# Kernel tuning notes

Hardware: AMD Instinct MI355X
Metric: run time of the kernel (lower is better)

## Reference

```python
import jax, jax.numpy as jnp
import numpy as np

N_NODES = 50000
N_EDGES = 400000
N_GRAPHS = 512
F = 32        # num_features
NB = 32       # mp_num_basis_fn
ZMAX = 118
CUTOFF = 5.0
NSPH = 9      # (mp_max_degree+1)^2 with max_degree=2
DEG_IDX = jnp.array([0, 1, 1, 1, 2, 2, 2, 2, 2])  # degree of each spherical component


def _bernstein(u, n=NB):
    # reciprocal_bernstein radial basis: Bernstein polynomials of degree n-1 at u in [0,1)
    k = jnp.arange(n, dtype=jnp.float32)
    log_binom = (jax.scipy.special.gammaln(float(n)) - jax.scipy.special.gammaln(k + 1.0)
                 - jax.scipy.special.gammaln(float(n) - k))
    u = jnp.clip(u, 1e-7, 1.0 - 1e-7)[..., None]
    return jnp.exp(log_binom + k * jnp.log(u) + (float(n) - 1.0 - k) * jnp.log1p(-u))


def _smooth_cutoff(r, cutoff=CUTOFF):
    t = r / cutoff
    return jnp.where(t < 1.0, jnp.exp(1.0 - 1.0 / jnp.clip(1.0 - t * t, 1e-7, None)), 0.0)


def _sph(u):
    # real spherical harmonics (cartesian normalization) up to degree 2; u: (E,3) unit vectors
    x, y, z = u[:, 0], u[:, 1], u[:, 2]
    c = jnp.sqrt(jnp.float32(3.0))
    return jnp.stack([jnp.ones_like(x), y, z, x,
                      c * x * y, c * y * z, 0.5 * (3.0 * z * z - 1.0),
                      c * z * x, 0.5 * c * (x * x - y * y)], axis=-1)


def _dense(x, W, b):
    # equivariant Dense: shared kernel over spherical components, bias only on scalar (l=0)
    y = jnp.einsum('nmf,fg->nmg', x, W)
    return y.at[:, 0, :].add(b)


def _silu_gate(x):
    # equivariant silu: scalar channel gates all degrees (scalar part -> exact silu)
    return x * jax.nn.sigmoid(x[:, 0:1, :])


def setup_inputs() -> dict:
    key = jax.random.key(0)
    ks = jax.random.split(key, 24)
    s = 1.0 / np.sqrt(F)
    sb = 1.0 / np.sqrt(NB)
    inp = {
        'positions': 2.0 * jax.random.normal(ks[0], (N_NODES, 3), jnp.float32),
        'embed': jax.random.normal(ks[1], (ZMAX, F), jnp.float32),
        'Wy0': sb * jax.random.normal(ks[2], (3, NB, F), jnp.float32),
        'Wx0': sb * jax.random.normal(ks[3], (3, NB, F), jnp.float32),
        'W1_0': s * jax.random.normal(ks[4], (F, F), jnp.float32),
        'b1_0': jnp.zeros((F,), jnp.float32),
        'W2_0': s * jax.random.normal(ks[5], (F, F), jnp.float32),
        'b2_0': jnp.zeros((F,), jnp.float32),
        'c0': jnp.full((1,), 0.5, jnp.float32),
        'Wr_last': sb * jax.random.normal(ks[6], (NB, F), jnp.float32),
        'W1_1': s * jax.random.normal(ks[7], (F, F), jnp.float32),
        'b1_1': jnp.zeros((F,), jnp.float32),
        'W2_1': s * jax.random.normal(ks[8], (F, F), jnp.float32),
        'b2_1': jnp.zeros((F,), jnp.float32),
        'c1': jnp.full((1,), 0.5, jnp.float32),
        'Wro1': s * jax.random.normal(ks[9], (F, F), jnp.float32),
        'bro1': jnp.zeros((F,), jnp.float32),
        'Wro2': s * jax.random.normal(ks[10], (F, 1), jnp.float32),
        'bro2': jnp.zeros((1,), jnp.float32),
        'atomic_bias': jax.random.normal(ks[11], (ZMAX,), jnp.float32),
        'atomic_numbers': jax.random.randint(ks[12], (N_NODES,), 0, ZMAX, jnp.int32),
        'dst_idx': jax.random.randint(ks[13], (N_EDGES,), 0, N_NODES, jnp.int32),
        'src_idx': jax.random.randint(ks[14], (N_EDGES,), 0, N_NODES, jnp.int32),
        'batch_segments': jnp.sort(jax.random.randint(ks[15], (N_NODES,), 0, N_GRAPHS, jnp.int32)),
        'graph_mask': jnp.ones((N_GRAPHS,), jnp.bool_),
    }
    return inp


def reference(positions, embed, Wy0, Wx0, W1_0, b1_0, W2_0, b2_0, c0,
              Wr_last, W1_1, b1_1, W2_1, b2_1, c1,
              Wro1, bro1, Wro2, bro2, atomic_bias,
              atomic_numbers, dst_idx, src_idx, batch_segments, graph_mask):
    # --- edge geometry (gather_src/gather_dst) ---
    disp = positions[src_idx] - positions[dst_idx]                # (E,3)
    r = jnp.sqrt(jnp.sum(disp * disp, axis=-1) + 1e-12)           # (E,)
    u = disp / r[:, None]
    Y = _sph(u)                                                   # (E,9)
    rbf = _bernstein(r / (r + 1.0)) * _smooth_cutoff(r)[:, None]  # (E,NB)

    # --- atomic embedding, lifted to (N, 9, F) with zero higher degrees ---
    x0 = embed[atomic_numbers]                                    # (N,F)
    x = jnp.concatenate([x0[:, None, :], jnp.zeros((N_NODES, NSPH - 1, F), x0.dtype)], axis=1)

    # --- iteration 0: full-degree equivariant message pass ---
    wy = jnp.einsum('eb,lbf->elf', rbf, Wy0)[:, DEG_IDX, :]       # (E,9,F) radial weights, (0,l)->l path
    wx = jnp.einsum('eb,lbf->elf', rbf, Wx0)[:, DEG_IDX, :]       # (l,0)->l path
    xs = x[src_idx]                                               # (E,9,F)
    msg = wy * Y[:, :, None] * xs[:, 0:1, :] + wx * xs
    y = jax.ops.segment_sum(msg, dst_idx, num_segments=N_NODES)   # (N,9,F)
    y = x + y
    y = _silu_gate(_dense(y, W1_0, b1_0))
    y = _dense(y, W2_0, b2_0)
    x = x + jax.nn.silu(c0) * y                                   # y_nl == 0 (era disabled)

    # --- iteration 1 (last): max_degree=0 message pass, then reduce to scalars ---
    w0 = rbf @ Wr_last                                            # (E,F)
    msg0 = w0 * x[src_idx, 0, :]
    y0 = jax.ops.segment_sum(msg0, dst_idx, num_segments=N_NODES) # (N,F)
    xs0 = x[:, 0, :]                                              # change_max_degree -> scalars
    y0 = xs0 + y0
    y0 = jax.nn.silu(y0 @ W1_1 + b1_1)
    y0 = y0 @ W2_1 + b2_1
    xs0 = xs0 + jax.nn.silu(c1) * y0

    # --- atomic readout and per-graph sum ---
    h = jax.nn.silu(xs0 @ Wro1 + bro1)
    e_atom = (h @ Wro2)[:, 0] + bro2[0] + atomic_bias[atomic_numbers]
    e_graph = jax.ops.segment_sum(e_atom, batch_segments, num_segments=N_GRAPHS)
    return jnp.where(graph_mask, e_graph, 0.0)
```

## Files before the change

kernel.cpp:

```cpp
#include <hip/hip_runtime.h>
#include <math.h>

#define NNODES 50000
#define NEDGES 400000
#define NGRAPHS 512
#define FDIM 32
#define CAP 32

static constexpr float BINOM31[32] = {
    1.f, 31.f, 465.f, 4495.f, 31465.f, 169911.f, 736281.f, 2629575.f,
    7888725.f, 20160075.f, 44352165.f, 84672315.f, 141120525.f, 206253075.f,
    265182525.f, 300540195.f, 300540195.f, 265182525.f, 206253075.f,
    141120525.f, 84672315.f, 44352165.f, 20160075.f, 7888725.f, 2629575.f,
    736281.f, 169911.f, 31465.f, 4495.f, 465.f, 31.f, 1.f
};

__device__ __forceinline__ float fast_rcp(float x) {
    return __builtin_amdgcn_rcpf(x);
}
__device__ __forceinline__ float silu(float x) {
    return x * fast_rcp(1.0f + __expf(-x));
}

__global__ __launch_bounds__(256) void prep(
    const float* __restrict__ pos,
    const float* __restrict__ Wy0, const float* __restrict__ Wx0,
    const float* __restrict__ Wr_last,
    float4* __restrict__ pos4, int* __restrict__ deg,
    float* __restrict__ out,
    float* __restrict__ cwA, float* __restrict__ cwB)
{
    int i = blockIdx.x * 256 + threadIdx.x;
    if (i < NGRAPHS) out[i] = 0.0f;
    if (i < FDIM * FDIM) {
        float b = BINOM31[i >> 5];
        cwA[i] = b * (Wy0[i] + Wx0[i]);
        cwB[i] = b * Wr_last[i];
    }
    if (i < NNODES) {
        pos4[i] = make_float4(pos[3 * i], pos[3 * i + 1], pos[3 * i + 2], 0.f);
        deg[i] = 0;
    }
}

__global__ __launch_bounds__(256) void build_csr(
    const float4* __restrict__ pos4,
    const int* __restrict__ srci, const int* __restrict__ dsti,
    const int* __restrict__ Z,
    float4* __restrict__ pay, int* __restrict__ deg)
{
    int e = blockIdx.x * 256 + threadIdx.x;
    if (e >= NEDGES) return;
    int s = srci[e], d = dsti[e];
    float4 ps = pos4[s];
    float4 pd = pos4[d];
    float dx = ps.x - pd.x, dy = ps.y - pd.y, dz = ps.z - pd.z;
    float r = sqrtf(dx * dx + dy * dy + dz * dz + 1e-12f);
    if (r >= 5.0f) return;

    float t = r * 0.2f;
    float q = fmaxf(1.0f - t * t, 1e-7f);
    float cut = __expf(1.0f - fast_rcp(q));
    float v = fast_rcp(r + 1.0f);
    float v2 = v * v, v4 = v2 * v2, v8 = v4 * v4, v16 = v8 * v8;
    float scale = v16 * v8 * v4 * v2 * v * cut;

    int rank = atomicAdd(&deg[d], 1);
    if (rank < CAP)
        pay[(size_t)d * CAP + rank] =
            make_float4(r, scale,
                        __int_as_float(s * FDIM),
                        __int_as_float(Z[s] * FDIM));
}

__global__ __launch_bounds__(256) void pad_slots(
    float4* __restrict__ pay, int* __restrict__ deg)
{
    int n = blockIdx.x * 256 + threadIdx.x;
    if (n >= NNODES) return;
    int d = min(deg[n], CAP);
    int dr = (d + 1) & ~1;
    float4 zf = make_float4(0.f, 0.f, 0.f, 0.f);
    for (int j = d; j < dr; ++j) pay[(size_t)n * CAP + j] = zf;
    deg[n] = dr;
}

#define DECLC(CW, K) float C##K = (CW)[(K) * FDIM + f];
#define DECL_ALL_C(CW)                                                      \
    DECLC(CW,0)  DECLC(CW,1)  DECLC(CW,2)  DECLC(CW,3)  DECLC(CW,4)        \
    DECLC(CW,5)  DECLC(CW,6)  DECLC(CW,7)  DECLC(CW,8)  DECLC(CW,9)        \
    DECLC(CW,10) DECLC(CW,11) DECLC(CW,12) DECLC(CW,13) DECLC(CW,14)       \
    DECLC(CW,15) DECLC(CW,16) DECLC(CW,17) DECLC(CW,18) DECLC(CW,19)       \
    DECLC(CW,20) DECLC(CW,21) DECLC(CW,22) DECLC(CW,23) DECLC(CW,24)       \
    DECLC(CW,25) DECLC(CW,26) DECLC(CW,27) DECLC(CW,28) DECLC(CW,29)       \
    DECLC(CW,30) DECLC(CW,31)

#define HEO(KE, KO)                                                        \
    _ea = fmaf(_ea, _r2a, C##KE); _oa = fmaf(_oa, _r2a, C##KO);            \
    _eb = fmaf(_eb, _r2b, C##KE); _ob = fmaf(_ob, _r2b, C##KO);

#define GATHER_PIPE(ACC, XSRC, ROWSEL)                                     \
    float ACC = 0.0f;                                                      \
    if (dgr > 0) {                                                         \
        float4 _pa = _h0, _pb = _h1;                                       \
        for (int j = 0; ; j += 2) {                                        \
            float _xa = (XSRC)[__float_as_int(_pa.ROWSEL) + f];            \
            float _xb = (XSRC)[__float_as_int(_pb.ROWSEL) + f];            \
            float4 _na = slot[j + 2];                                      \
            float4 _nb = slot[j + 3];                                      \
            float _r2a = _pa.x * _pa.x, _r2b = _pb.x * _pb.x;              \
            float _ea = C30, _oa = C31, _eb = C30, _ob = C31;              \
            HEO(28, 29) HEO(26, 27) HEO(24, 25) HEO(22, 23) HEO(20, 21)   \
            HEO(18, 19) HEO(16, 17) HEO(14, 15) HEO(12, 13) HEO(10, 11)   \
            HEO(8, 9)   HEO(6, 7)   HEO(4, 5)   HEO(2, 3)   HEO(0, 1)     \
            float _wa = fmaf(_pa.x, _oa, _ea);                             \
            float _wb = fmaf(_pb.x, _ob, _eb);                             \
            ACC = fmaf(_pa.y * _wa, _xa, ACC);                             \
            ACC = fmaf(_pb.y * _wb, _xb, ACC);                             \
            if (j + 2 >= dgr) break;                                       \
            _pa = _na; _pb = _nb;                                          \
        }                                                                  \
    }

#define MATVEC32L(RES, WL, YP, BIAS) do {                                  \
    float4 _q0=(YP)[0], _q1=(YP)[1], _q2=(YP)[2], _q3=(YP)[3];             \
    float4 _q4=(YP)[4], _q5=(YP)[5], _q6=(YP)[6], _q7=(YP)[7];             \
    float _a0=(BIAS), _a1=0.f, _a2=0.f, _a3=0.f;                           \
    _a0=fmaf(_q0.x,(WL)[ 0*FDIM+f],_a0); _a0=fmaf(_q0.y,(WL)[ 1*FDIM+f],_a0); \
    _a0=fmaf(_q0.z,(WL)[ 2*FDIM+f],_a0); _a0=fmaf(_q0.w,(WL)[ 3*FDIM+f],_a0); \
    _a1=fmaf(_q1.x,(WL)[ 4*FDIM+f],_a1); _a1=fmaf(_q1.y,(WL)[ 5*FDIM+f],_a1); \
    _a1=fmaf(_q1.z,(WL)[ 6*FDIM+f],_a1); _a1=fmaf(_q1.w,(WL)[ 7*FDIM+f],_a1); \
    _a2=fmaf(_q2.x,(WL)[ 8*FDIM+f],_a2); _a2=fmaf(_q2.y,(WL)[ 9*FDIM+f],_a2); \
    _a2=fmaf(_q2.z,(WL)[10*FDIM+f],_a2); _a2=fmaf(_q2.w,(WL)[11*FDIM+f],_a2); \
    _a3=fmaf(_q3.x,(WL)[12*FDIM+f],_a3); _a3=fmaf(_q3.y,(WL)[13*FDIM+f],_a3); \
    _a3=fmaf(_q3.z,(WL)[14*FDIM+f],_a3); _a3=fmaf(_q3.w,(WL)[15*FDIM+f],_a3); \
    _a0=fmaf(_q4.x,(WL)[16*FDIM+f],_a0); _a0=fmaf(_q4.y,(WL)[17*FDIM+f],_a0); \
    _a0=fmaf(_q4.z,(WL)[18*FDIM+f],_a0); _a0=fmaf(_q4.w,(WL)[19*FDIM+f],_a0); \
    _a1=fmaf(_q5.x,(WL)[20*FDIM+f],_a1); _a1=fmaf(_q5.y,(WL)[21*FDIM+f],_a1); \
    _a1=fmaf(_q5.z,(WL)[22*FDIM+f],_a1); _a1=fmaf(_q5.w,(WL)[23*FDIM+f],_a1); \
    _a2=fmaf(_q6.x,(WL)[24*FDIM+f],_a2); _a2=fmaf(_q6.y,(WL)[25*FDIM+f],_a2); \
    _a2=fmaf(_q6.z,(WL)[26*FDIM+f],_a2); _a2=fmaf(_q6.w,(WL)[27*FDIM+f],_a2); \
    _a3=fmaf(_q7.x,(WL)[28*FDIM+f],_a3); _a3=fmaf(_q7.y,(WL)[29*FDIM+f],_a3); \
    _a3=fmaf(_q7.z,(WL)[30*FDIM+f],_a3); _a3=fmaf(_q7.w,(WL)[31*FDIM+f],_a3); \
    RES = (_a0+_a1)+(_a2+_a3); } while (0)

__global__ __launch_bounds__(256, 7) void fused_a(
    const float4* __restrict__ pay, const int* __restrict__ deg,
    const float* __restrict__ embed, const int* __restrict__ Z,
    const float* __restrict__ cwA,
    const float* __restrict__ W1, const float* __restrict__ b1,
    const float* __restrict__ W2, const float* __restrict__ b2,
    const float* __restrict__ c0,
    float* __restrict__ x1buf)
{
    __shared__ __align__(16) float ylds[4][64];
    int tid = threadIdx.x;
    int widx = tid >> 6;
    int lane = tid & 63;
    int f    = lane & 31;
    int half = lane >> 5;

    int n = (blockIdx.x * 4 + widx) * 2 + half;
    const float4* slot = pay + (size_t)n * CAP;
    int dgr = deg[n];
    float4 _h0 = slot[0], _h1 = slot[1];
    float x0 = embed[Z[n] * FDIM + f];
    DECL_ALL_C(cwA)

    GATHER_PIPE(accv, embed, w)

    float yv = x0 + accv;

    float* yrow = &ylds[widx][half * 32];
    const float4* yp = (const float4*)yrow;
    yrow[f] = yv;
    float t;
    MATVEC32L(t, W1, yp, b1[f]);
    t = silu(t);
    yrow[f] = t;
    float u;
    MATVEC32L(u, W2, yp, b2[f]);
    x1buf[(size_t)n * FDIM + f] = fmaf(silu(c0[0]), u, x0);
}

__global__ __launch_bounds__(256, 7) void fused_b(
    const float4* __restrict__ pay, const int* __restrict__ deg,
    const float* __restrict__ x1buf, const float* __restrict__ cwB,
    const float* __restrict__ W1, const float* __restrict__ b1,
    const float* __restrict__ W2, const float* __restrict__ b2,
    const float* __restrict__ c1,
    const float* __restrict__ Wro1, const float* __restrict__ bro1,
    const float* __restrict__ Wro2, const float* __restrict__ bro2,
    const float* __restrict__ abias, const int* __restrict__ Z,
    const int* __restrict__ segs,
    float* __restrict__ out)
{
    __shared__ __align__(16) float ylds[4][64];
    __shared__ float eb[8];
    __shared__ int   sb[8];
    int tid = threadIdx.x;
    int widx = tid >> 6;
    int lane = tid & 63;
    int f    = lane & 31;
    int half = lane >> 5;

    int n = (blockIdx.x * 4 + widx) * 2 + half;
    const float4* slot = pay + (size_t)n * CAP;
    int dgr = deg[n];
    float4 _h0 = slot[0], _h1 = slot[1];
    float x1 = x1buf[(size_t)n * FDIM + f];
    int   zn = Z[n];
    DECL_ALL_C(cwB)

    GATHER_PIPE(accv, x1buf, z)

    float yv = x1 + accv;

    float* yrow = &ylds[widx][half * 32];
    const float4* yp = (const float4*)yrow;
    yrow[f] = yv;
    float t;
    MATVEC32L(t, W1, yp, b1[f]);
    t = silu(t);
    yrow[f] = t;
    float u;
    MATVEC32L(u, W2, yp, b2[f]);
    float xs0 = fmaf(silu(c1[0]), u, x1);
    yrow[f] = xs0;
    float h;
    MATVEC32L(h, Wro1, yp, bro1[f]);
    float p = silu(h) * Wro2[f];
    p += __shfl_xor(p, 16, 32);
    p += __shfl_xor(p, 8, 32);
    p += __shfl_xor(p, 4, 32);
    p += __shfl_xor(p, 2, 32);
    p += __shfl_xor(p, 1, 32);

    if (f == 0) {
        eb[widx * 2 + half] = p + bro2[0] + abias[zn];
        sb[widx * 2 + half] = segs[n];
    }
    __syncthreads();
    if (tid == 0) {
        float acc = eb[0];
        int cur = sb[0];
        #pragma unroll
        for (int i = 1; i < 8; ++i) {
            if (sb[i] == cur) acc += eb[i];
            else { atomicAdd(&out[cur], acc); cur = sb[i]; acc = eb[i]; }
        }
        atomicAdd(&out[cur], acc);
    }
}

extern "C" void kernel_launch(void* const* d_in, const int* in_sizes, int n_in,
                              void* d_out, int out_size, void* d_ws, size_t ws_size,
                              hipStream_t stream)
{
    const float* pos     = (const float*)d_in[0];
    const float* embed   = (const float*)d_in[1];
    const float* Wy0     = (const float*)d_in[2];
    const float* Wx0     = (const float*)d_in[3];
    const float* W1_0    = (const float*)d_in[4];
    const float* b1_0    = (const float*)d_in[5];
    const float* W2_0    = (const float*)d_in[6];
    const float* b2_0    = (const float*)d_in[7];
    const float* c0      = (const float*)d_in[8];
    const float* Wr_last = (const float*)d_in[9];
    const float* W1_1    = (const float*)d_in[10];
    const float* b1_1    = (const float*)d_in[11];
    const float* W2_1    = (const float*)d_in[12];
    const float* b2_1    = (const float*)d_in[13];
    const float* c1      = (const float*)d_in[14];
    const float* Wro1    = (const float*)d_in[15];
    const float* bro1    = (const float*)d_in[16];
    const float* Wro2    = (const float*)d_in[17];
    const float* bro2    = (const float*)d_in[18];
    const float* abias   = (const float*)d_in[19];
    const int*   Z       = (const int*)d_in[20];
    const int*   dsti    = (const int*)d_in[21];
    const int*   srci    = (const int*)d_in[22];
    const int*   segs    = (const int*)d_in[23];

    float* out = (float*)d_out;

    char* w = (char*)d_ws;
    float4* pay   = (float4*)w;  w += (size_t)NNODES * CAP * 16;
    float*  x1buf = (float*)w;   w += (size_t)NNODES * FDIM * 4;
    float4* pos4  = (float4*)w;  w += (size_t)NNODES * 16;
    int*    deg   = (int*)w;     w += (size_t)NNODES * 4;
    float*  cwA   = (float*)w;   w += FDIM * FDIM * 4;
    float*  cwB   = (float*)w;   w += FDIM * FDIM * 4;

    const int edgeBlocks = (NEDGES + 255) / 256;
    const int nodeBlocks = NNODES / 8;
    const int prepBlocks = (NNODES + 255) / 256;

    prep<<<prepBlocks, 256, 0, stream>>>(pos, Wy0, Wx0, Wr_last,
                                         pos4, deg, out, cwA, cwB);
    build_csr<<<edgeBlocks, 256, 0, stream>>>(pos4, srci, dsti, Z, pay, deg);
    pad_slots<<<prepBlocks, 256, 0, stream>>>(pay, deg);
    fused_a<<<nodeBlocks, 256, 0, stream>>>(pay, deg, embed, Z, cwA,
                                            W1_0, b1_0, W2_0, b2_0, c0, x1buf);
    fused_b<<<nodeBlocks, 256, 0, stream>>>(pay, deg, x1buf, cwB,
                                            W1_1, b1_1, W2_1, b2_1, c1,
                                            Wro1, bro1, Wro2, bro2,
                                            abias, Z, segs, out);
}
```

Baseline: 194.8 us.

## Move radial coefficients and dense weights to LDS and drop prep/pad kernels

Per-thread register copies of the 32 Bernstein-scaled radial coefficients are replaced by a per-block LDS table in float2 even/odd layout. W1/W2/Wro1 are also staged into LDS, and occupancy is raised from 7 to 8 blocks via launch bounds. The prep and pad_slots kernels are removed: position reads go straight to the strided pos array, zeroing uses hipMemsetAsync on deg, out and the whole payload buffer, and odd-degree rounding moves into the fused kernels. The trade-offs are extra LDS reads in the inner Horner loop, per-block redundant weight preparation, and a full memset of the large payload buffer.

```diff
diff --git a/kernel.cpp b/kernel.cpp
--- a/kernel.cpp
+++ b/kernel.cpp
@@ -7,7 +7,7 @@
 #define FDIM 32
 #define CAP 32
 
-static constexpr float BINOM31[32] = {
+static __device__ const float BINOM31[32] = {
     1.f, 31.f, 465.f, 4495.f, 31465.f, 169911.f, 736281.f, 2629575.f,
     7888725.f, 20160075.f, 44352165.f, 84672315.f, 141120525.f, 206253075.f,
     265182525.f, 300540195.f, 300540195.f, 265182525.f, 206253075.f,
@@ -22,29 +22,8 @@
     return x * fast_rcp(1.0f + __expf(-x));
 }
 
-__global__ __launch_bounds__(256) void prep(
+__global__ __launch_bounds__(256) void build_csr(
     const float* __restrict__ pos,
-    const float* __restrict__ Wy0, const float* __restrict__ Wx0,
-    const float* __restrict__ Wr_last,
-    float4* __restrict__ pos4, int* __restrict__ deg,
-    float* __restrict__ out,
-    float* __restrict__ cwA, float* __restrict__ cwB)
-{
-    int i = blockIdx.x * 256 + threadIdx.x;
-    if (i < NGRAPHS) out[i] = 0.0f;
-    if (i < FDIM * FDIM) {
-        float b = BINOM31[i >> 5];
-        cwA[i] = b * (Wy0[i] + Wx0[i]);
-        cwB[i] = b * Wr_last[i];
-    }
-    if (i < NNODES) {
-        pos4[i] = make_float4(pos[3 * i], pos[3 * i + 1], pos[3 * i + 2], 0.f);
-        deg[i] = 0;
-    }
-}
-
-__global__ __launch_bounds__(256) void build_csr(
-    const float4* __restrict__ pos4,
     const int* __restrict__ srci, const int* __restrict__ dsti,
     const int* __restrict__ Z,
     float4* __restrict__ pay, int* __restrict__ deg)
@@ -52,9 +31,9 @@
     int e = blockIdx.x * 256 + threadIdx.x;
     if (e >= NEDGES) return;
     int s = srci[e], d = dsti[e];
-    float4 ps = pos4[s];
-    float4 pd = pos4[d];
-    float dx = ps.x - pd.x, dy = ps.y - pd.y, dz = ps.z - pd.z;
+    float dx = pos[3 * s]     - pos[3 * d];
+    float dy = pos[3 * s + 1] - pos[3 * d + 1];
+    float dz = pos[3 * s + 2] - pos[3 * d + 2];
     float r = sqrtf(dx * dx + dy * dy + dz * dz + 1e-12f);
     if (r >= 5.0f) return;
 
@@ -73,46 +52,28 @@
                         __int_as_float(Z[s] * FDIM));
 }
 
-__global__ __launch_bounds__(256) void pad_slots(
-    float4* __restrict__ pay, int* __restrict__ deg)
-{
-    int n = blockIdx.x * 256 + threadIdx.x;
-    if (n >= NNODES) return;
-    int d = min(deg[n], CAP);
-    int dr = (d + 1) & ~1;
-    float4 zf = make_float4(0.f, 0.f, 0.f, 0.f);
-    for (int j = d; j < dr; ++j) pay[(size_t)n * CAP + j] = zf;
-    deg[n] = dr;
-}
-
-#define DECLC(CW, K) float C##K = (CW)[(K) * FDIM + f];
-#define DECL_ALL_C(CW)                                                      \
-    DECLC(CW,0)  DECLC(CW,1)  DECLC(CW,2)  DECLC(CW,3)  DECLC(CW,4)        \
-    DECLC(CW,5)  DECLC(CW,6)  DECLC(CW,7)  DECLC(CW,8)  DECLC(CW,9)        \
-    DECLC(CW,10) DECLC(CW,11) DECLC(CW,12) DECLC(CW,13) DECLC(CW,14)       \
-    DECLC(CW,15) DECLC(CW,16) DECLC(CW,17) DECLC(CW,18) DECLC(CW,19)       \
-    DECLC(CW,20) DECLC(CW,21) DECLC(CW,22) DECLC(CW,23) DECLC(CW,24)       \
-    DECLC(CW,25) DECLC(CW,26) DECLC(CW,27) DECLC(CW,28) DECLC(CW,29)       \
-    DECLC(CW,30) DECLC(CW,31)
-
-#define HEO(KE, KO)                                                        \
-    _ea = fmaf(_ea, _r2a, C##KE); _oa = fmaf(_oa, _r2a, C##KO);            \
-    _eb = fmaf(_eb, _r2b, C##KE); _ob = fmaf(_ob, _r2b, C##KO);
-
-#define GATHER_PIPE(ACC, XSRC, ROWSEL)                                     \
+#define GATHER_PIPE(ACC, XSRC, ROWSEL, CWL)                                \
     float ACC = 0.0f;                                                      \
     if (dgr > 0) {                                                         \
         float4 _pa = _h0, _pb = _h1;                                       \
+        const float2* _cw = (const float2*)((CWL) + (f << 1));             \
         for (int j = 0; ; j += 2) {                                        \
             float _xa = (XSRC)[__float_as_int(_pa.ROWSEL) + f];            \
             float _xb = (XSRC)[__float_as_int(_pb.ROWSEL) + f];            \
             float4 _na = slot[j + 2];                                      \
             float4 _nb = slot[j + 3];                                      \
             float _r2a = _pa.x * _pa.x, _r2b = _pb.x * _pb.x;              \
-            float _ea = C30, _oa = C31, _eb = C30, _ob = C31;              \
-            HEO(28, 29) HEO(26, 27) HEO(24, 25) HEO(22, 23) HEO(20, 21)   \
-            HEO(18, 19) HEO(16, 17) HEO(14, 15) HEO(12, 13) HEO(10, 11)   \
-            HEO(8, 9)   HEO(6, 7)   HEO(4, 5)   HEO(2, 3)   HEO(0, 1)     \
+            float2 _c15 = _cw[15 * 32];                                    \
+            float _ea = _c15.x, _oa = _c15.y;                              \
+            float _eb = _c15.x, _ob = _c15.y;                              \
+            _Pragma("unroll")                                              \
+            for (int p = 14; p >= 0; --p) {                                \
+                float2 _cc = _cw[p * 32];                                  \
+                _ea = fmaf(_ea, _r2a, _cc.x);                              \
+                _oa = fmaf(_oa, _r2a, _cc.y);                              \
+                _eb = fmaf(_eb, _r2b, _cc.x);                              \
+                _ob = fmaf(_ob, _r2b, _cc.y);                              \
+            }                                                              \
             float _wa = fmaf(_pa.x, _oa, _ea);                             \
             float _wb = fmaf(_pb.x, _ob, _eb);                             \
             ACC = fmaf(_pa.y * _wa, _xa, ACC);                             \
@@ -144,16 +105,19 @@
     _a3=fmaf(_q7.z,(WL)[30*FDIM+f],_a3); _a3=fmaf(_q7.w,(WL)[31*FDIM+f],_a3); \
     RES = (_a0+_a1)+(_a2+_a3); } while (0)
 
-__global__ __launch_bounds__(256, 7) void fused_a(
+__global__ __launch_bounds__(256, 8) void fused_a(
     const float4* __restrict__ pay, const int* __restrict__ deg,
     const float* __restrict__ embed, const int* __restrict__ Z,
-    const float* __restrict__ cwA,
+    const float* __restrict__ Wy0, const float* __restrict__ Wx0,
     const float* __restrict__ W1, const float* __restrict__ b1,
     const float* __restrict__ W2, const float* __restrict__ b2,
     const float* __restrict__ c0,
     float* __restrict__ x1buf)
 {
     __shared__ __align__(16) float ylds[4][64];
+    __shared__ __align__(16) float cwl[FDIM * FDIM];
+    __shared__ __align__(16) float W1l[FDIM * FDIM];
+    __shared__ __align__(16) float W2l[FDIM * FDIM];
     int tid = threadIdx.x;
     int widx = tid >> 6;
     int lane = tid & 63;
@@ -162,12 +126,20 @@
 
     int n = (blockIdx.x * 4 + widx) * 2 + half;
     const float4* slot = pay + (size_t)n * CAP;
-    int dgr = deg[n];
+    int dgr = (min(deg[n], CAP) + 1) & ~1;
     float4 _h0 = slot[0], _h1 = slot[1];
     float x0 = embed[Z[n] * FDIM + f];
-    DECL_ALL_C(cwA)
-
-    GATHER_PIPE(accv, embed, w)
+
+    for (int i = tid; i < FDIM * FDIM; i += 256) {
+        int k = i >> 5, ff = i & 31;
+        cwl[(k >> 1) * 64 + (ff << 1) + (k & 1)] =
+            BINOM31[k] * (Wy0[i] + Wx0[i]);
+        W1l[i] = W1[i];
+        W2l[i] = W2[i];
+    }
+    __syncthreads();
+
+    GATHER_PIPE(accv, embed, w, cwl)
 
     float yv = x0 + accv;
 
@@ -175,17 +147,17 @@
     const float4* yp = (const float4*)yrow;
     yrow[f] = yv;
     float t;
-    MATVEC32L(t, W1, yp, b1[f]);
+    MATVEC32L(t, W1l, yp, b1[f]);
     t = silu(t);
     yrow[f] = t;
     float u;
-    MATVEC32L(u, W2, yp, b2[f]);
+    MATVEC32L(u, W2l, yp, b2[f]);
     x1buf[(size_t)n * FDIM + f] = fmaf(silu(c0[0]), u, x0);
 }
 
-__global__ __launch_bounds__(256, 7) void fused_b(
+__global__ __launch_bounds__(256, 8) void fused_b(
     const float4* __restrict__ pay, const int* __restrict__ deg,
-    const float* __restrict__ x1buf, const float* __restrict__ cwB,
+    const float* __restrict__ x1buf, const float* __restrict__ Wr_last,
     const float* __restrict__ W1, const float* __restrict__ b1,
     const float* __restrict__ W2, const float* __restrict__ b2,
     const float* __restrict__ c1,
@@ -196,6 +168,10 @@
     float* __restrict__ out)
 {
     __shared__ __align__(16) float ylds[4][64];
+    __shared__ __align__(16) float cwl[FDIM * FDIM];
+    __shared__ __align__(16) float W1l[FDIM * FDIM];
+    __shared__ __align__(16) float W2l[FDIM * FDIM];
+    __shared__ __align__(16) float Wrl[FDIM * FDIM];
     __shared__ float eb[8];
     __shared__ int   sb[8];
     int tid = threadIdx.x;
@@ -206,13 +182,21 @@
 
     int n = (blockIdx.x * 4 + widx) * 2 + half;
     const float4* slot = pay + (size_t)n * CAP;
-    int dgr = deg[n];
+    int dgr = (min(deg[n], CAP) + 1) & ~1;
     float4 _h0 = slot[0], _h1 = slot[1];
     float x1 = x1buf[(size_t)n * FDIM + f];
     int   zn = Z[n];
-    DECL_ALL_C(cwB)
-
-    GATHER_PIPE(accv, x1buf, z)
+
+    for (int i = tid; i < FDIM * FDIM; i += 256) {
+        int k = i >> 5, ff = i & 31;
+        cwl[(k >> 1) * 64 + (ff << 1) + (k & 1)] = BINOM31[k] * Wr_last[i];
+        W1l[i] = W1[i];
+        W2l[i] = W2[i];
+        Wrl[i] = Wro1[i];
+    }
+    __syncthreads();
+
+    GATHER_PIPE(accv, x1buf, z, cwl)
 
     float yv = x1 + accv;
 
@@ -220,15 +204,15 @@
     const float4* yp = (const float4*)yrow;
     yrow[f] = yv;
     float t;
-    MATVEC32L(t, W1, yp, b1[f]);
+    MATVEC32L(t, W1l, yp, b1[f]);
     t = silu(t);
     yrow[f] = t;
     float u;
-    MATVEC32L(u, W2, yp, b2[f]);
+    MATVEC32L(u, W2l, yp, b2[f]);
     float xs0 = fmaf(silu(c1[0]), u, x1);
     yrow[f] = xs0;
     float h;
-    MATVEC32L(h, Wro1, yp, bro1[f]);
+    MATVEC32L(h, Wrl, yp, bro1[f]);
     float p = silu(h) * Wro2[f];
     p += __shfl_xor(p, 16, 32);
     p += __shfl_xor(p, 8, 32);
@@ -287,22 +271,19 @@
     char* w = (char*)d_ws;
     float4* pay   = (float4*)w;  w += (size_t)NNODES * CAP * 16;
     float*  x1buf = (float*)w;   w += (size_t)NNODES * FDIM * 4;
-    float4* pos4  = (float4*)w;  w += (size_t)NNODES * 16;
     int*    deg   = (int*)w;     w += (size_t)NNODES * 4;
-    float*  cwA   = (float*)w;   w += FDIM * FDIM * 4;
-    float*  cwB   = (float*)w;   w += FDIM * FDIM * 4;
 
     const int edgeBlocks = (NEDGES + 255) / 256;
     const int nodeBlocks = NNODES / 8;
-    const int prepBlocks = (NNODES + 255) / 256;
-
-    prep<<<prepBlocks, 256, 0, stream>>>(pos, Wy0, Wx0, Wr_last,
-                                         pos4, deg, out, cwA, cwB);
-    build_csr<<<edgeBlocks, 256, 0, stream>>>(pos4, srci, dsti, Z, pay, deg);
-    pad_slots<<<prepBlocks, 256, 0, stream>>>(pay, deg);
-    fused_a<<<nodeBlocks, 256, 0, stream>>>(pay, deg, embed, Z, cwA,
+
+    hipMemsetAsync(pay, 0, (size_t)NNODES * CAP * 16, stream);
+    hipMemsetAsync(deg, 0, (size_t)NNODES * 4, stream);
+    hipMemsetAsync(out, 0, (size_t)NGRAPHS * 4, stream);
+
+    build_csr<<<edgeBlocks, 256, 0, stream>>>(pos, srci, dsti, Z, pay, deg);
+    fused_a<<<nodeBlocks, 256, 0, stream>>>(pay, deg, embed, Z, Wy0, Wx0,
                                             W1_0, b1_0, W2_0, b2_0, c0, x1buf);
-    fused_b<<<nodeBlocks, 256, 0, stream>>>(pay, deg, x1buf, cwB,
+    fused_b<<<nodeBlocks, 256, 0, stream>>>(pay, deg, x1buf, Wr_last,
                                             W1_1, b1_1, W2_1, b2_1, c1,
                                             Wro1, bro1, Wro2, bro2,
                                             abias, Z, segs, out);
```

After: 192.1 us. Within noise of the previous version (-1.4%).
